# Kernel tuning notes

Measured on AMD Instinct MI355X. Metric: run time of the kernel, lower is better.

## Reference

```python
import jax, jax.numpy as jnp
import numpy as np

D_MODEL = 96
N_HEAD = 3
HEAD_DIM = D_MODEL // N_HEAD  # 32
D_FF = 2048
WIDTH = 65
HALF_W = (WIDTH - 1) // 2  # 32
EPS = 1e-5


def layer_norm(x, g, b):
    mu = jnp.mean(x, axis=-1, keepdims=True)
    var = jnp.mean(jnp.square(x - mu), axis=-1, keepdims=True)
    return (x - mu) * jax.lax.rsqrt(var + EPS) * g + b


def setup_inputs() -> dict:
    key = jax.random.key(0)
    ks = jax.random.split(key, 8)
    B, T = 8, 2048
    s = 0.05
    return {
        "x": jax.random.normal(ks[0], (B, D_MODEL, T), dtype=jnp.float32),
        "w_qkv": jax.random.normal(ks[1], (3 * D_MODEL, D_MODEL), dtype=jnp.float32) * s,
        "b_qkv": jnp.zeros((3 * D_MODEL,), dtype=jnp.float32),
        "w_out": jax.random.normal(ks[2], (D_MODEL, D_MODEL), dtype=jnp.float32) * s,
        "b_out": jnp.zeros((D_MODEL,), dtype=jnp.float32),
        "ln1_g": jnp.ones((D_MODEL,), dtype=jnp.float32),
        "ln1_b": jnp.zeros((D_MODEL,), dtype=jnp.float32),
        "w_ff1": jax.random.normal(ks[3], (D_FF, D_MODEL), dtype=jnp.float32) * s,
        "b_ff1": jnp.zeros((D_FF,), dtype=jnp.float32),
        "w_ff2": jax.random.normal(ks[4], (D_MODEL, D_FF), dtype=jnp.float32) * s,
        "b_ff2": jnp.zeros((D_MODEL,), dtype=jnp.float32),
        "ln2_g": jnp.ones((D_MODEL,), dtype=jnp.float32),
        "ln2_b": jnp.zeros((D_MODEL,), dtype=jnp.float32),
        "lnf_g": jnp.ones((D_MODEL,), dtype=jnp.float32),
        "lnf_b": jnp.zeros((D_MODEL,), dtype=jnp.float32),
    }


def reference(x, w_qkv, b_qkv, w_out, b_out, ln1_g, ln1_b, w_ff1, b_ff1,
              w_ff2, b_ff2, ln2_g, ln2_b, lnf_g, lnf_b):
    # x: (B, C, T) -> (B, T, C)
    h = jnp.transpose(x, (0, 2, 1))
    B, T, C = h.shape

    # --- multi-head self-attention with banded mask ---
    qkv = h @ w_qkv.T + b_qkv                      # (B, T, 3C)
    q, k, v = jnp.split(qkv, 3, axis=-1)
    q = q.reshape(B, T, N_HEAD, HEAD_DIM)
    k = k.reshape(B, T, N_HEAD, HEAD_DIM)
    v = v.reshape(B, T, N_HEAD, HEAD_DIM)

    scale = 1.0 / jnp.sqrt(jnp.float32(HEAD_DIM))
    scores = jnp.einsum("bthd,bshd->bhts", q, k) * scale  # (B, H, T, T)

    idx = jnp.arange(T)
    band = jnp.abs(idx[:, None] - idx[None, :]) <= HALF_W  # |i-j| <= half width
    scores = jnp.where(band[None, None], scores, jnp.float32(-jnp.inf))

    attn = jax.nn.softmax(scores, axis=-1)
    ctx = jnp.einsum("bhts,bshd->bthd", attn, v).reshape(B, T, C)
    attn_out = ctx @ w_out.T + b_out

    # --- post-norm encoder layer (dropout inactive / eval mode) ---
    h = layer_norm(h + attn_out, ln1_g, ln1_b)
    ff = jax.nn.relu(h @ w_ff1.T + b_ff1) @ w_ff2.T + b_ff2
    h = layer_norm(h + ff, ln2_g, ln2_b)

    # extra layernorm applied when width is not None
    h = layer_norm(h, lnf_g, lnf_b)

    # (B, T, C) -> (B, C, T)
    return jnp.transpose(h, (0, 2, 1))
```

## Files before the change

kernel.cpp:

```cpp
#include <hip/hip_runtime.h>
#include <hip/hip_bf16.h>

#define B 8
#define T 2048
#define C 96
#define NH 3
#define HD 32
#define FFD 2048
#define HALF_W 32
#define BT (B*T)

typedef __hip_bfloat16 bf16;
typedef __attribute__((ext_vector_type(8))) short short8;
typedef __attribute__((ext_vector_type(4))) short short4v;
typedef __attribute__((ext_vector_type(16))) float floatx16;

__device__ __forceinline__ short f2bs(float v){
    __hip_bfloat16 h = __float2bfloat16(v);
    return *reinterpret_cast<short*>(&h);
}
__device__ __forceinline__ float bs2f(short s){
    unsigned u = ((unsigned)(unsigned short)s) << 16;
    return __uint_as_float(u);
}
__device__ __forceinline__ short8 ld_b64x2(const short* p){
    short4v a = *(const short4v*)p;
    short4v b = *(const short4v*)(p + 4);
    short8 v;
    v[0]=a[0]; v[1]=a[1]; v[2]=a[2]; v[3]=a[3];
    v[4]=b[0]; v[5]=b[1]; v[6]=b[2]; v[7]=b[3];
    return v;
}
__device__ __forceinline__ int4 exch_pair(int a0,int a1,int b0,int b1,int hq){
    int ra0=__shfl_xor(a0,32), ra1=__shfl_xor(a1,32);
    int rb0=__shfl_xor(b0,32), rb1=__shfl_xor(b1,32);
    int4 s;
    s.x = hq ? rb0 : a0;
    s.y = hq ? rb1 : a1;
    s.z = hq ? b0  : ra0;
    s.w = hq ? b1  : ra1;
    return s;
}
__device__ __forceinline__ void proj_pack(const floatx16& acc, const float* bias32, int hq,
                                          short8& f0, short8& f1){
    int pkq[4][2];
    #pragma unroll
    for(int q = 0; q < 4; ++q){
        float4 bv = *(const float4*)(bias32 + 8*q + 4*hq);
        short4v t;
        t[0]=f2bs(acc[4*q+0]+bv.x); t[1]=f2bs(acc[4*q+1]+bv.y);
        t[2]=f2bs(acc[4*q+2]+bv.z); t[3]=f2bs(acc[4*q+3]+bv.w);
        int2 u = *(int2*)&t; pkq[q][0]=u.x; pkq[q][1]=u.y;
    }
    int4 r0 = exch_pair(pkq[0][0],pkq[0][1],pkq[1][0],pkq[1][1],hq);
    int4 r1 = exch_pair(pkq[2][0],pkq[2][1],pkq[3][0],pkq[3][1],hq);
    f0 = *(short8*)&r0; f1 = *(short8*)&r1;
}

__global__ void cvtw_kernel(const float* __restrict__ wq, const float* __restrict__ wo,
                            const float* __restrict__ w1, const float* __restrict__ w2,
                            bf16* __restrict__ dst){
    int i = blockIdx.x*256 + threadIdx.x;
    if(i < 27648){
        int e = i&7, lane = (i>>3)&63, r = i>>9;
        int ks = r%6, ot = r/6;
        int o = ot*32 + (lane&31);
        int k = ks*16 + (lane>>5)*8 + e;
        dst[i] = __float2bfloat16(wq[o*96 + k]);
    } else if(i < 36864){
        int j = i - 27648;
        int e = j&7, lane = (j>>3)&63, r = j>>9;
        int ks = r%6, ct = r/6;
        int c = ct*32 + (lane&31);
        int k = ks*16 + (lane>>5)*8 + e;
        dst[i] = __float2bfloat16(wo[c*96 + k]);
    } else if(i < 233472){
        int j = i - 36864;
        int e = j&7, lane = (j>>3)&63, r = j>>9;
        int ks = r%6; r /= 6;
        int w = r%4, jt = r/4;
        int row = jt*128 + w*32 + (lane&31);
        int k = ks*16 + (lane>>5)*8 + e;
        dst[i] = __float2bfloat16(w1[row*96 + k]);
    } else if(i < 430080){
        int j = i - 233472;
        int e = j&7, lane = (j>>3)&63, r = j>>9;
        int ct = r%3; r /= 3;
        int g = r%2; r /= 2;
        int w = r%4, jt = r/4;
        int c = ct*32 + (lane&31);
        int k = jt*128 + w*32 + g*16 + (lane>>5)*8 + e;
        dst[i] = __float2bfloat16(w2[c*FFD + k]);
    }
}

__global__ __launch_bounds__(192, 2) void encoder_kernel(
    const float* __restrict__ x,
    const bf16* __restrict__ wqs, const bf16* __restrict__ wos,
    const bf16* __restrict__ w1s, const bf16* __restrict__ w2s,
    const float* __restrict__ b_qkv, const float* __restrict__ b_out,
    const float* __restrict__ g1, const float* __restrict__ bb1,
    const float* __restrict__ b1, const float* __restrict__ b2,
    const float* __restrict__ g2, const float* __restrict__ bt2,
    const float* __restrict__ gf, const float* __restrict__ btf,
    float* __restrict__ out){
    __shared__ __align__(16) char smem[73088];
    float* XS   = (float*)smem;
    short* PTS  = (short*)smem;
    float* REDP = (float*)smem;
    short* VTS  = (short*)(smem + 39936);
    float* ZT   = (float*)(smem + 39936);
    short* CTX  = (short*)(smem + 59136);
    short* H1S  = (short*)(smem + 65536);
    float* LSS  = (float*)(smem + 71936);
    float* RED1 = (float*)(smem + 72320);

    const int tid = threadIdx.x;
    const int w = tid / 64, lane = tid & 63;
    const int lm = lane & 31, hq = lane >> 5;
    const int b  = blockIdx.x >> 6;
    const int tt = blockIdx.x & 63;
    const int t0 = tt * 32;
    const float* xb = x + (size_t)b*C*T;

    short8 wof[6];
    #pragma unroll
    for(int ks = 0; ks < 6; ++ks)
        wof[ks] = *(const short8*)((const short*)wos + (size_t)(w*6 + ks)*512 + lane*8);

    int tg0 = t0 - 32;
    if(tg0 >= 0 && t0 + 64 <= T){
        for(int e = tid; e < 96*24; e += 192){
            int c = e / 24, q4 = e % 24;
            *(float4*)(XS + c*104 + q4*4) = *(const float4*)(xb + (size_t)c*T + tg0 + q4*4);
        }
    } else {
        for(int e = tid; e < 96*96; e += 192){
            int c = e / 96, j = e % 96;
            int t = tg0 + j; t = t < 0 ? 0 : (t > T-1 ? T-1 : t);
            XS[c*104 + j] = xb[(size_t)c*T + t];
        }
    }
    __syncthreads();

    short8 kwf[6], vwf[6];
    #pragma unroll
    for(int ks = 0; ks < 6; ++ks){
        kwf[ks] = *(const short8*)((const short*)wqs + (size_t)((3+w)*6 + ks)*512 + lane*8);
        vwf[ks] = *(const short8*)((const short*)wqs + (size_t)((6+w)*6 + ks)*512 + lane*8);
    }
    short8 kf[3][2]; short8 qf0, qf1;
    #pragma unroll
    for(int tau = 0; tau < 3; ++tau){
        short8 bfr[6];
        #pragma unroll
        for(int ks = 0; ks < 6; ++ks){
            short8 vv;
            #pragma unroll
            for(int i = 0; i < 8; ++i)
                vv[i] = f2bs(XS[(ks*16 + hq*8 + i)*104 + tau*32 + lm]);
            bfr[ks] = vv;
        }
        floatx16 acc;
        #pragma unroll
        for(int r = 0; r < 16; ++r) acc[r] = 0.f;
        #pragma unroll
        for(int ks = 0; ks < 6; ++ks)
            acc = __builtin_amdgcn_mfma_f32_32x32x16_bf16(kwf[ks], bfr[ks], acc, 0,0,0);
        proj_pack(acc, b_qkv + (3+w)*32, hq, kf[tau][0], kf[tau][1]);
        #pragma unroll
        for(int r = 0; r < 16; ++r) acc[r] = 0.f;
        #pragma unroll
        for(int ks = 0; ks < 6; ++ks)
            acc = __builtin_amdgcn_mfma_f32_32x32x16_bf16(vwf[ks], bfr[ks], acc, 0,0,0);
        #pragma unroll
        for(int q = 0; q < 4; ++q){
            float4 bv = *(const float4*)(b_qkv + (6+w)*32 + 8*q + 4*hq);
            float bva[4] = {bv.x, bv.y, bv.z, bv.w};
            #pragma unroll
            for(int r = 0; r < 4; ++r)
                VTS[w*3200 + (8*q + 4*hq + r)*100 + tau*32 + lm] = f2bs(acc[4*q+r] + bva[r]);
        }
        if(tau == 1){
            floatx16 qa;
            #pragma unroll
            for(int r = 0; r < 16; ++r) qa[r] = 0.f;
            #pragma unroll
            for(int ks = 0; ks < 6; ++ks){
                short8 qwf = *(const short8*)((const short*)wqs + (size_t)(w*6 + ks)*512 + lane*8);
                qa = __builtin_amdgcn_mfma_f32_32x32x16_bf16(qwf, bfr[ks], qa, 0,0,0);
            }
            proj_pack(qa, b_qkv + w*32, hq, qf0, qf1);
        }
    }
    __syncthreads();

    floatx16 S[3];
    #pragma unroll
    for(int sub = 0; sub < 3; ++sub){
        floatx16 z;
        #pragma unroll
        for(int r = 0; r < 16; ++r) z[r] = 0.f;
        z = __builtin_amdgcn_mfma_f32_32x32x16_bf16(kf[sub][0], qf0, z, 0,0,0);
        z = __builtin_amdgcn_mfma_f32_32x32x16_bf16(kf[sub][1], qf1, z, 0,0,0);
        S[sub] = z;
    }
    const float scale = 0.17677669529663687f;
    float part = 0.f;
    #pragma unroll
    for(int sub = 0; sub < 3; ++sub){
        #pragma unroll
        for(int r = 0; r < 16; ++r){
            int key_local = sub*32 + (r&3) + 8*(r>>2) + 4*hq;
            int s_glob = t0 - 32 + key_local;
            int rel = key_local - lm;
            bool ok = (rel >= 0) && (rel <= 64) && (s_glob >= 0) && (s_glob < T);
            float p = ok ? __expf(S[sub][r]*scale) : 0.f;
            S[sub][r] = p;
            part += p;
        }
    }
    float ltot = part + __shfl_xor(part, 32);
    if(hq == 0) LSS[w*32 + lm] = ltot;
    #pragma unroll
    for(int sub = 0; sub < 3; ++sub){
        #pragma unroll
        for(int q4 = 0; q4 < 4; ++q4){
            int kbase = sub*32 + 8*q4 + 4*hq;
            short4v pk4;
            pk4[0] = f2bs(S[sub][4*q4+0]);
            pk4[1] = f2bs(S[sub][4*q4+1]);
            pk4[2] = f2bs(S[sub][4*q4+2]);
            pk4[3] = f2bs(S[sub][4*q4+3]);
            *(short4v*)(PTS + w*3200 + lm*100 + kbase) = pk4;
        }
    }
    floatx16 O;
    #pragma unroll
    for(int r = 0; r < 16; ++r) O[r] = 0.f;
    #pragma unroll
    for(int ks = 0; ks < 6; ++ks){
        short8 pa = ld_b64x2(PTS + w*3200 + lm*100 + ks*16 + hq*8);
        short8 vf = ld_b64x2(VTS + w*3200 + lm*100 + ks*16 + hq*8);
        O = __builtin_amdgcn_mfma_f32_32x32x16_bf16(pa, vf, O, 0,0,0);
    }
    #pragma unroll
    for(int r = 0; r < 16; ++r){
        int qr = (r&3) + 8*(r>>2) + 4*hq;
        float linv = 1.f / LSS[w*32 + qr];
        CTX[qr*100 + w*32 + lm] = f2bs(O[r]*linv);
    }
    __syncthreads();

    short8 cbfr[6];
    #pragma unroll
    for(int ks = 0; ks < 6; ++ks)
        cbfr[ks] = ld_b64x2(CTX + lm*100 + ks*16 + hq*8);
    floatx16 pacc;
    #pragma unroll
    for(int r = 0; r < 16; ++r) pacc[r] = 0.f;
    #pragma unroll
    for(int ks = 0; ks < 6; ++ks)
        pacc = __builtin_amdgcn_mfma_f32_32x32x16_bf16(wof[ks], cbfr[ks], pacc, 0,0,0);
    float vals[16];
    float p1 = 0.f, p2 = 0.f;
    #pragma unroll
    for(int q = 0; q < 4; ++q){
        int c = w*32 + 8*q + 4*hq;
        float4 bv = *(const float4*)(b_out + c);
        float bva[4] = {bv.x, bv.y, bv.z, bv.w};
        #pragma unroll
        for(int r = 0; r < 4; ++r){
            float xv = xb[(size_t)(c + r)*T + t0 + lm];
            float v = pacc[4*q+r] + bva[r] + xv;
            vals[4*q+r] = v;
            p1 += v; p2 += v*v;
        }
    }
    p1 += __shfl_xor(p1, 32);
    p2 += __shfl_xor(p2, 32);
    if(hq == 0){ RED1[w*32 + lm] = p1; RED1[96 + w*32 + lm] = p2; }
    __syncthreads();
    {
        float s  = RED1[lm] + RED1[32 + lm] + RED1[64 + lm];
        float s2 = RED1[96 + lm] + RED1[128 + lm] + RED1[160 + lm];
        float mu = s * (1.0f/96.0f);
        float rstd = rsqrtf(s2*(1.0f/96.0f) - mu*mu + 1e-5f);
        #pragma unroll
        for(int q = 0; q < 4; ++q){
            int c = w*32 + 8*q + 4*hq;
            float4 gv = *(const float4*)(g1 + c);
            float4 bv = *(const float4*)(bb1 + c);
            float ga[4] = {gv.x, gv.y, gv.z, gv.w};
            float ba[4] = {bv.x, bv.y, bv.z, bv.w};
            short4v pkv;
            #pragma unroll
            for(int r = 0; r < 4; ++r)
                pkv[r] = f2bs((vals[4*q+r] - mu)*rstd*ga[r] + ba[r]);
            *(short4v*)(H1S + lm*100 + c) = pkv;
        }
    }
    __syncthreads();

    short8 hf[6];
    #pragma unroll
    for(int ks = 0; ks < 6; ++ks)
        hf[ks] = ld_b64x2(H1S + lm*100 + ks*16 + hq*8);
    floatx16 acc2[3];
    #pragma unroll
    for(int i = 0; i < 3; ++i)
        #pragma unroll
        for(int r = 0; r < 16; ++r) acc2[i][r] = 0.f;
    const short* w1b = (const short*)w1s + lane*8;
    const short* w2b = (const short*)w2s + lane*8;
    short8 cw1[6], cw2[6];
    #pragma unroll
    for(int ks = 0; ks < 6; ++ks)
        cw1[ks] = *(const short8*)(w1b + (size_t)(w*6 + ks)*512);
    #pragma unroll
    for(int g = 0; g < 2; ++g)
        #pragma unroll
        for(int ct = 0; ct < 3; ++ct)
            cw2[g*3 + ct] = *(const short8*)(w2b + (size_t)((w*2 + g)*3 + ct)*512);
    for(int J = w; J < 64; J += 3){
        int Jn = (J + 3 < 64) ? J + 3 : w;
        short8 nw1[6], nw2[6];
        #pragma unroll
        for(int ks = 0; ks < 6; ++ks)
            nw1[ks] = *(const short8*)(w1b + (size_t)(Jn*6 + ks)*512);
        #pragma unroll
        for(int g = 0; g < 2; ++g)
            #pragma unroll
            for(int ct = 0; ct < 3; ++ct)
                nw2[g*3 + ct] = *(const short8*)(w2b + (size_t)((Jn*2 + g)*3 + ct)*512);
        floatx16 a0;
        #pragma unroll
        for(int r = 0; r < 16; ++r) a0[r] = 0.f;
        #pragma unroll
        for(int ks = 0; ks < 6; ++ks)
            a0 = __builtin_amdgcn_mfma_f32_32x32x16_bf16(cw1[ks], hf[ks], a0, 0,0,0);
        int pk[4][2];
        #pragma unroll
        for(int q = 0; q < 4; ++q){
            float4 bv = *(const float4*)(b1 + J*32 + 8*q + 4*hq);
            float bva[4] = {bv.x, bv.y, bv.z, bv.w};
            short4v tv;
            #pragma unroll
            for(int r = 0; r < 4; ++r){
                float v0 = a0[4*q+r] + bva[r];
                tv[r] = f2bs(v0 > 0.f ? v0 : 0.f);
            }
            int2 u = *(int2*)&tv; pk[q][0] = u.x; pk[q][1] = u.y;
        }
        #pragma unroll
        for(int g = 0; g < 2; ++g){
            int4 sfi = exch_pair(pk[2*g][0], pk[2*g][1], pk[2*g+1][0], pk[2*g+1][1], hq);
            short8 sf = *(short8*)&sfi;
            #pragma unroll
            for(int ct = 0; ct < 3; ++ct)
                acc2[ct] = __builtin_amdgcn_mfma_f32_32x32x16_bf16(cw2[g*3+ct], sf, acc2[ct], 0,0,0);
        }
        #pragma unroll
        for(int ks = 0; ks < 6; ++ks) cw1[ks] = nw1[ks];
        #pragma unroll
        for(int i = 0; i < 6; ++i) cw2[i] = nw2[i];
    }
    #pragma unroll
    for(int ct = 0; ct < 3; ++ct)
        #pragma unroll
        for(int q = 0; q < 4; ++q)
            #pragma unroll
            for(int r = 0; r < 4; ++r)
                REDP[(w*3 + ct)*1088 + lane*17 + 4*q + r] = acc2[ct][4*q+r];
    __syncthreads();

    float fv[16];
    float e1 = 0.f, e2 = 0.f;
    #pragma unroll
    for(int q = 0; q < 4; ++q){
        int c = w*32 + 8*q + 4*hq;
        float4 bv = *(const float4*)(b2 + c);
        float bva[4] = {bv.x, bv.y, bv.z, bv.w};
        #pragma unroll
        for(int r = 0; r < 4; ++r){
            float v = REDP[(0 + w)*1088 + lane*17 + 4*q + r]
                    + REDP[(3 + w)*1088 + lane*17 + 4*q + r]
                    + REDP[(6 + w)*1088 + lane*17 + 4*q + r]
                    + bva[r] + bs2f(H1S[lm*100 + c + r]);
            fv[4*q+r] = v;
            e1 += v; e2 += v*v;
        }
    }
    e1 += __shfl_xor(e1, 32);
    e2 += __shfl_xor(e2, 32);
    if(hq == 0){ RED1[w*32 + lm] = e1; RED1[96 + w*32 + lm] = e2; }
    __syncthreads();
    float f1 = 0.f, f2 = 0.f;
    {
        float s  = RED1[lm] + RED1[32 + lm] + RED1[64 + lm];
        float s2 = RED1[96 + lm] + RED1[128 + lm] + RED1[160 + lm];
        float mu = s * (1.0f/96.0f);
        float rstd = rsqrtf(s2*(1.0f/96.0f) - mu*mu + 1e-5f);
        #pragma unroll
        for(int q = 0; q < 4; ++q){
            int c = w*32 + 8*q + 4*hq;
            float4 gv = *(const float4*)(g2 + c);
            float4 bv = *(const float4*)(bt2 + c);
            float ga[4] = {gv.x, gv.y, gv.z, gv.w};
            float ba[4] = {bv.x, bv.y, bv.z, bv.w};
            #pragma unroll
            for(int r = 0; r < 4; ++r){
                float y = (fv[4*q+r] - mu)*rstd*ga[r] + ba[r];
                fv[4*q+r] = y;
                f1 += y; f2 += y*y;
            }
        }
    }
    f1 += __shfl_xor(f1, 32);
    f2 += __shfl_xor(f2, 32);
    __syncthreads();
    if(hq == 0){ RED1[w*32 + lm] = f1; RED1[96 + w*32 + lm] = f2; }
    __syncthreads();
    {
        float s  = RED1[lm] + RED1[32 + lm] + RED1[64 + lm];
        float s2 = RED1[96 + lm] + RED1[128 + lm] + RED1[160 + lm];
        float mu = s * (1.0f/96.0f);
        float rstd = rsqrtf(s2*(1.0f/96.0f) - mu*mu + 1e-5f);
        #pragma unroll
        for(int q = 0; q < 4; ++q){
            int c = w*32 + 8*q + 4*hq;
            float4 gv = *(const float4*)(gf + c);
            float4 bv = *(const float4*)(btf + c);
            float ga[4] = {gv.x, gv.y, gv.z, gv.w};
            float ba[4] = {bv.x, bv.y, bv.z, bv.w};
            #pragma unroll
            for(int r = 0; r < 4; ++r)
                ZT[(c + r)*36 + lm] = (fv[4*q+r] - mu)*rstd*ga[r] + ba[r];
        }
    }
    __syncthreads();
    float* ob = out + (size_t)b*C*T + t0;
    for(int e = tid; e < 96*8; e += 192){
        int c = e >> 3, qq = e & 7;
        *(float4*)(ob + (size_t)c*T + qq*4) = *(const float4*)(ZT + c*36 + qq*4);
    }
}

extern "C" void kernel_launch(void* const* d_in, const int* in_sizes, int n_in,
                              void* d_out, int out_size, void* d_ws, size_t ws_size,
                              hipStream_t stream) {
    const float* x     = (const float*)d_in[0];
    const float* w_qkv = (const float*)d_in[1];
    const float* b_qkv = (const float*)d_in[2];
    const float* w_out = (const float*)d_in[3];
    const float* b_out = (const float*)d_in[4];
    const float* ln1_g = (const float*)d_in[5];
    const float* ln1_b = (const float*)d_in[6];
    const float* w_ff1 = (const float*)d_in[7];
    const float* b_ff1 = (const float*)d_in[8];
    const float* w_ff2 = (const float*)d_in[9];
    const float* b_ff2 = (const float*)d_in[10];
    const float* ln2_g = (const float*)d_in[11];
    const float* ln2_b = (const float*)d_in[12];
    const float* lnf_g = (const float*)d_in[13];
    const float* lnf_b = (const float*)d_in[14];
    float* out = (float*)d_out;

    bf16* wts = (bf16*)d_ws;
    bf16* wqs = wts;
    bf16* wos = wts + 27648;
    bf16* w1s = wts + 36864;
    bf16* w2s = wts + 233472;

    cvtw_kernel   <<<1680, 256, 0, stream>>>(w_qkv, w_out, w_ff1, w_ff2, wts);
    encoder_kernel<<<B*(T/32), 192, 0, stream>>>(x, wqs, wos, w1s, w2s,
                                                 b_qkv, b_out, ln1_g, ln1_b,
                                                 b_ff1, b_ff2, ln2_g, ln2_b,
                                                 lnf_g, lnf_b, out);
}
```

Measured before the change: 124.6 us.

## Double block to six waves, split K/V projection and FFN chunks across waves

Raises the block size from 3 to 6 wavefronts. In the projection stage, three waves compute Q/K and three compute V. All six waves share the FFN hidden-chunk loop, and the six partial FFN2 accumulators are reduced through shared memory one channel tile at a time. X is staged in LDS as bf16 in time-major layout so MFMA operands load as vectors, which shrinks shared memory. This adds more barriers and leaves half the waves idle during attention and the layernorms, in exchange for more waves to hide latency in the FFN-dominated section.

```diff
diff --git a/kernel.cpp b/kernel.cpp
--- a/kernel.cpp
+++ b/kernel.cpp
@@ -9,6 +9,7 @@
 #define FFD 2048
 #define HALF_W 32
 #define BT (B*T)
+#define NT 384
 
 typedef __hip_bfloat16 bf16;
 typedef __attribute__((ext_vector_type(8))) short short8;
@@ -94,7 +95,7 @@
     }
 }
 
-__global__ __launch_bounds__(192, 2) void encoder_kernel(
+__global__ __launch_bounds__(384, 3) void encoder_kernel(
     const float* __restrict__ x,
     const bf16* __restrict__ wqs, const bf16* __restrict__ wos,
     const bf16* __restrict__ w1s, const bf16* __restrict__ w2s,
@@ -104,191 +105,206 @@
     const float* __restrict__ g2, const float* __restrict__ bt2,
     const float* __restrict__ gf, const float* __restrict__ btf,
     float* __restrict__ out){
-    __shared__ __align__(16) char smem[73088];
-    float* XS   = (float*)smem;
+    __shared__ __align__(16) char smem[59392];
+    short* XS   = (short*)smem;
     short* PTS  = (short*)smem;
     float* REDP = (float*)smem;
-    short* VTS  = (short*)(smem + 39936);
-    float* ZT   = (float*)(smem + 39936);
-    short* CTX  = (short*)(smem + 59136);
-    short* H1S  = (short*)(smem + 65536);
-    float* LSS  = (float*)(smem + 71936);
-    float* RED1 = (float*)(smem + 72320);
+    short* VTS  = (short*)(smem + 26112);
+    float* ZT   = (float*)(smem + 26112);
+    short* CTX  = (short*)(smem + 45312);
+    short* H1S  = (short*)(smem + 51712);
+    float* LSS  = (float*)(smem + 58112);
+    float* RED1 = (float*)(smem + 58496);
 
     const int tid = threadIdx.x;
-    const int w = tid / 64, lane = tid & 63;
+    const int u = tid >> 6, lane = tid & 63;
     const int lm = lane & 31, hq = lane >> 5;
+    const int grp = u / 3, h = u % 3;
     const int b  = blockIdx.x >> 6;
     const int tt = blockIdx.x & 63;
     const int t0 = tt * 32;
     const float* xb = x + (size_t)b*C*T;
 
-    short8 wof[6];
-    #pragma unroll
-    for(int ks = 0; ks < 6; ++ks)
-        wof[ks] = *(const short8*)((const short*)wos + (size_t)(w*6 + ks)*512 + lane*8);
-
     int tg0 = t0 - 32;
     if(tg0 >= 0 && t0 + 64 <= T){
-        for(int e = tid; e < 96*24; e += 192){
-            int c = e / 24, q4 = e % 24;
-            *(float4*)(XS + c*104 + q4*4) = *(const float4*)(xb + (size_t)c*T + tg0 + q4*4);
+        for(int e = tid; e < 96*24; e += NT){
+            int c = e / 24, t4 = e % 24;
+            float4 v = *(const float4*)(xb + (size_t)c*T + tg0 + t4*4);
+            XS[(t4*4+0)*104 + c] = f2bs(v.x);
+            XS[(t4*4+1)*104 + c] = f2bs(v.y);
+            XS[(t4*4+2)*104 + c] = f2bs(v.z);
+            XS[(t4*4+3)*104 + c] = f2bs(v.w);
         }
     } else {
-        for(int e = tid; e < 96*96; e += 192){
+        for(int e = tid; e < 96*96; e += NT){
             int c = e / 96, j = e % 96;
             int t = tg0 + j; t = t < 0 ? 0 : (t > T-1 ? T-1 : t);
-            XS[c*104 + j] = xb[(size_t)c*T + t];
-        }
-    }
-    __syncthreads();
-
-    short8 kwf[6], vwf[6];
-    #pragma unroll
-    for(int ks = 0; ks < 6; ++ks){
-        kwf[ks] = *(const short8*)((const short*)wqs + (size_t)((3+w)*6 + ks)*512 + lane*8);
-        vwf[ks] = *(const short8*)((const short*)wqs + (size_t)((6+w)*6 + ks)*512 + lane*8);
-    }
-    short8 kf[3][2]; short8 qf0, qf1;
-    #pragma unroll
-    for(int tau = 0; tau < 3; ++tau){
-        short8 bfr[6];
+            XS[j*104 + c] = f2bs(xb[(size_t)c*T + t]);
+        }
+    }
+    __syncthreads();
+
+    short8 kf[3][2], qf0, qf1, wof[6];
+    if(grp == 0){
+        short8 kwf[6];
+        #pragma unroll
+        for(int ks = 0; ks < 6; ++ks)
+            kwf[ks] = *(const short8*)((const short*)wqs + (size_t)((3+h)*6 + ks)*512 + lane*8);
+        #pragma unroll
+        for(int tau = 0; tau < 3; ++tau){
+            short8 bfr[6];
+            #pragma unroll
+            for(int ks = 0; ks < 6; ++ks)
+                bfr[ks] = *(const short8*)(XS + (tau*32+lm)*104 + ks*16 + hq*8);
+            floatx16 acc;
+            #pragma unroll
+            for(int r = 0; r < 16; ++r) acc[r] = 0.f;
+            #pragma unroll
+            for(int ks = 0; ks < 6; ++ks)
+                acc = __builtin_amdgcn_mfma_f32_32x32x16_bf16(kwf[ks], bfr[ks], acc, 0,0,0);
+            proj_pack(acc, b_qkv + (3+h)*32, hq, kf[tau][0], kf[tau][1]);
+            if(tau == 1){
+                floatx16 qa;
+                #pragma unroll
+                for(int r = 0; r < 16; ++r) qa[r] = 0.f;
+                #pragma unroll
+                for(int ks = 0; ks < 6; ++ks){
+                    short8 qwf = *(const short8*)((const short*)wqs + (size_t)(h*6 + ks)*512 + lane*8);
+                    qa = __builtin_amdgcn_mfma_f32_32x32x16_bf16(qwf, bfr[ks], qa, 0,0,0);
+                }
+                proj_pack(qa, b_qkv + h*32, hq, qf0, qf1);
+            }
+        }
+        #pragma unroll
+        for(int ks = 0; ks < 6; ++ks)
+            wof[ks] = *(const short8*)((const short*)wos + (size_t)(h*6 + ks)*512 + lane*8);
+    } else {
+        short8 vwf[6];
+        #pragma unroll
+        for(int ks = 0; ks < 6; ++ks)
+            vwf[ks] = *(const short8*)((const short*)wqs + (size_t)((6+h)*6 + ks)*512 + lane*8);
+        #pragma unroll
+        for(int tau = 0; tau < 3; ++tau){
+            short8 bfr[6];
+            #pragma unroll
+            for(int ks = 0; ks < 6; ++ks)
+                bfr[ks] = *(const short8*)(XS + (tau*32+lm)*104 + ks*16 + hq*8);
+            floatx16 acc;
+            #pragma unroll
+            for(int r = 0; r < 16; ++r) acc[r] = 0.f;
+            #pragma unroll
+            for(int ks = 0; ks < 6; ++ks)
+                acc = __builtin_amdgcn_mfma_f32_32x32x16_bf16(vwf[ks], bfr[ks], acc, 0,0,0);
+            #pragma unroll
+            for(int q = 0; q < 4; ++q){
+                float4 bv = *(const float4*)(b_qkv + (6+h)*32 + 8*q + 4*hq);
+                float bva[4] = {bv.x, bv.y, bv.z, bv.w};
+                #pragma unroll
+                for(int r = 0; r < 4; ++r)
+                    VTS[h*3200 + (8*q + 4*hq + r)*100 + tau*32 + lm] = f2bs(acc[4*q+r] + bva[r]);
+            }
+        }
+    }
+    __syncthreads();
+
+    if(grp == 0){
+        floatx16 S[3];
+        #pragma unroll
+        for(int sub = 0; sub < 3; ++sub){
+            floatx16 z;
+            #pragma unroll
+            for(int r = 0; r < 16; ++r) z[r] = 0.f;
+            z = __builtin_amdgcn_mfma_f32_32x32x16_bf16(kf[sub][0], qf0, z, 0,0,0);
+            z = __builtin_amdgcn_mfma_f32_32x32x16_bf16(kf[sub][1], qf1, z, 0,0,0);
+            S[sub] = z;
+        }
+        const float scale = 0.17677669529663687f;
+        float part = 0.f;
+        #pragma unroll
+        for(int sub = 0; sub < 3; ++sub){
+            #pragma unroll
+            for(int r = 0; r < 16; ++r){
+                int key_local = sub*32 + (r&3) + 8*(r>>2) + 4*hq;
+                int s_glob = t0 - 32 + key_local;
+                int rel = key_local - lm;
+                bool ok = (rel >= 0) && (rel <= 64) && (s_glob >= 0) && (s_glob < T);
+                float p = ok ? __expf(S[sub][r]*scale) : 0.f;
+                S[sub][r] = p;
+                part += p;
+            }
+        }
+        float ltot = part + __shfl_xor(part, 32);
+        if(hq == 0) LSS[h*32 + lm] = ltot;
+        #pragma unroll
+        for(int sub = 0; sub < 3; ++sub){
+            #pragma unroll
+            for(int q4 = 0; q4 < 4; ++q4){
+                int kbase = sub*32 + 8*q4 + 4*hq;
+                short4v pk4;
+                pk4[0] = f2bs(S[sub][4*q4+0]);
+                pk4[1] = f2bs(S[sub][4*q4+1]);
+                pk4[2] = f2bs(S[sub][4*q4+2]);
+                pk4[3] = f2bs(S[sub][4*q4+3]);
+                *(short4v*)(PTS + h*3200 + lm*100 + kbase) = pk4;
+            }
+        }
+        floatx16 O;
+        #pragma unroll
+        for(int r = 0; r < 16; ++r) O[r] = 0.f;
         #pragma unroll
         for(int ks = 0; ks < 6; ++ks){
-            short8 vv;
-            #pragma unroll
-            for(int i = 0; i < 8; ++i)
-                vv[i] = f2bs(XS[(ks*16 + hq*8 + i)*104 + tau*32 + lm]);
-            bfr[ks] = vv;
-        }
-        floatx16 acc;
-        #pragma unroll
-        for(int r = 0; r < 16; ++r) acc[r] = 0.f;
-        #pragma unroll
-        for(int ks = 0; ks < 6; ++ks)
-            acc = __builtin_amdgcn_mfma_f32_32x32x16_bf16(kwf[ks], bfr[ks], acc, 0,0,0);
-        proj_pack(acc, b_qkv + (3+w)*32, hq, kf[tau][0], kf[tau][1]);
-        #pragma unroll
-        for(int r = 0; r < 16; ++r) acc[r] = 0.f;
-        #pragma unroll
-        for(int ks = 0; ks < 6; ++ks)
-            acc = __builtin_amdgcn_mfma_f32_32x32x16_bf16(vwf[ks], bfr[ks], acc, 0,0,0);
+            short8 pa = ld_b64x2(PTS + h*3200 + lm*100 + ks*16 + hq*8);
+            short8 vf = ld_b64x2(VTS + h*3200 + lm*100 + ks*16 + hq*8);
+            O = __builtin_amdgcn_mfma_f32_32x32x16_bf16(pa, vf, O, 0,0,0);
+        }
+        #pragma unroll
+        for(int r = 0; r < 16; ++r){
+            int qr = (r&3) + 8*(r>>2) + 4*hq;
+            float linv = 1.f / LSS[h*32 + qr];
+            CTX[qr*100 + h*32 + lm] = f2bs(O[r]*linv);
+        }
+    }
+    __syncthreads();
+
+    float vals[16];
+    if(grp == 0){
+        short8 cbfr[6];
+        #pragma unroll
+        for(int ks = 0; ks < 6; ++ks)
+            cbfr[ks] = ld_b64x2(CTX + lm*100 + ks*16 + hq*8);
+        floatx16 pacc;
+        #pragma unroll
+        for(int r = 0; r < 16; ++r) pacc[r] = 0.f;
+        #pragma unroll
+        for(int ks = 0; ks < 6; ++ks)
+            pacc = __builtin_amdgcn_mfma_f32_32x32x16_bf16(wof[ks], cbfr[ks], pacc, 0,0,0);
+        float p1 = 0.f, p2 = 0.f;
         #pragma unroll
         for(int q = 0; q < 4; ++q){
-            float4 bv = *(const float4*)(b_qkv + (6+w)*32 + 8*q + 4*hq);
+            int c = h*32 + 8*q + 4*hq;
+            float4 bv = *(const float4*)(b_out + c);
             float bva[4] = {bv.x, bv.y, bv.z, bv.w};
             #pragma unroll
-            for(int r = 0; r < 4; ++r)
-                VTS[w*3200 + (8*q + 4*hq + r)*100 + tau*32 + lm] = f2bs(acc[4*q+r] + bva[r]);
-        }
-        if(tau == 1){
-            floatx16 qa;
-            #pragma unroll
-            for(int r = 0; r < 16; ++r) qa[r] = 0.f;
-            #pragma unroll
-            for(int ks = 0; ks < 6; ++ks){
-                short8 qwf = *(const short8*)((const short*)wqs + (size_t)(w*6 + ks)*512 + lane*8);
-                qa = __builtin_amdgcn_mfma_f32_32x32x16_bf16(qwf, bfr[ks], qa, 0,0,0);
-            }
-            proj_pack(qa, b_qkv + w*32, hq, qf0, qf1);
-        }
-    }
-    __syncthreads();
-
-    floatx16 S[3];
-    #pragma unroll
-    for(int sub = 0; sub < 3; ++sub){
-        floatx16 z;
-        #pragma unroll
-        for(int r = 0; r < 16; ++r) z[r] = 0.f;
-        z = __builtin_amdgcn_mfma_f32_32x32x16_bf16(kf[sub][0], qf0, z, 0,0,0);
-        z = __builtin_amdgcn_mfma_f32_32x32x16_bf16(kf[sub][1], qf1, z, 0,0,0);
-        S[sub] = z;
-    }
-    const float scale = 0.17677669529663687f;
-    float part = 0.f;
-    #pragma unroll
-    for(int sub = 0; sub < 3; ++sub){
-        #pragma unroll
-        for(int r = 0; r < 16; ++r){
-            int key_local = sub*32 + (r&3) + 8*(r>>2) + 4*hq;
-            int s_glob = t0 - 32 + key_local;
-            int rel = key_local - lm;
-            bool ok = (rel >= 0) && (rel <= 64) && (s_glob >= 0) && (s_glob < T);
-            float p = ok ? __expf(S[sub][r]*scale) : 0.f;
-            S[sub][r] = p;
-            part += p;
-        }
-    }
-    float ltot = part + __shfl_xor(part, 32);
-    if(hq == 0) LSS[w*32 + lm] = ltot;
-    #pragma unroll
-    for(int sub = 0; sub < 3; ++sub){
-        #pragma unroll
-        for(int q4 = 0; q4 < 4; ++q4){
-            int kbase = sub*32 + 8*q4 + 4*hq;
-            short4v pk4;
-            pk4[0] = f2bs(S[sub][4*q4+0]);
-            pk4[1] = f2bs(S[sub][4*q4+1]);
-            pk4[2] = f2bs(S[sub][4*q4+2]);
-            pk4[3] = f2bs(S[sub][4*q4+3]);
-            *(short4v*)(PTS + w*3200 + lm*100 + kbase) = pk4;
-        }
-    }
-    floatx16 O;
-    #pragma unroll
-    for(int r = 0; r < 16; ++r) O[r] = 0.f;
-    #pragma unroll
-    for(int ks = 0; ks < 6; ++ks){
-        short8 pa = ld_b64x2(PTS + w*3200 + lm*100 + ks*16 + hq*8);
-        short8 vf = ld_b64x2(VTS + w*3200 + lm*100 + ks*16 + hq*8);
-        O = __builtin_amdgcn_mfma_f32_32x32x16_bf16(pa, vf, O, 0,0,0);
-    }
-    #pragma unroll
-    for(int r = 0; r < 16; ++r){
-        int qr = (r&3) + 8*(r>>2) + 4*hq;
-        float linv = 1.f / LSS[w*32 + qr];
-        CTX[qr*100 + w*32 + lm] = f2bs(O[r]*linv);
-    }
-    __syncthreads();
-
-    short8 cbfr[6];
-    #pragma unroll
-    for(int ks = 0; ks < 6; ++ks)
-        cbfr[ks] = ld_b64x2(CTX + lm*100 + ks*16 + hq*8);
-    floatx16 pacc;
-    #pragma unroll
-    for(int r = 0; r < 16; ++r) pacc[r] = 0.f;
-    #pragma unroll
-    for(int ks = 0; ks < 6; ++ks)
-        pacc = __builtin_amdgcn_mfma_f32_32x32x16_bf16(wof[ks], cbfr[ks], pacc, 0,0,0);
-    float vals[16];
-    float p1 = 0.f, p2 = 0.f;
-    #pragma unroll
-    for(int q = 0; q < 4; ++q){
-        int c = w*32 + 8*q + 4*hq;
-        float4 bv = *(const float4*)(b_out + c);
-        float bva[4] = {bv.x, bv.y, bv.z, bv.w};
-        #pragma unroll
-        for(int r = 0; r < 4; ++r){
-            float xv = xb[(size_t)(c + r)*T + t0 + lm];
-            float v = pacc[4*q+r] + bva[r] + xv;
-            vals[4*q+r] = v;
-            p1 += v; p2 += v*v;
-        }
-    }
-    p1 += __shfl_xor(p1, 32);
-    p2 += __shfl_xor(p2, 32);
-    if(hq == 0){ RED1[w*32 + lm] = p1; RED1[96 + w*32 + lm] = p2; }
-    __syncthreads();
-    {
+            for(int r = 0; r < 4; ++r){
+                float xv = xb[(size_t)(c + r)*T + t0 + lm];
+                float v = pacc[4*q+r] + bva[r] + xv;
+                vals[4*q+r] = v;
+                p1 += v; p2 += v*v;
+            }
+        }
+        p1 += __shfl_xor(p1, 32);
+        p2 += __shfl_xor(p2, 32);
+        if(hq == 0){ RED1[h*32 + lm] = p1; RED1[96 + h*32 + lm] = p2; }
+    }
+    __syncthreads();
+    if(grp == 0){
         float s  = RED1[lm] + RED1[32 + lm] + RED1[64 + lm];
         float s2 = RED1[96 + lm] + RED1[128 + lm] + RED1[160 + lm];
         float mu = s * (1.0f/96.0f);
         float rstd = rsqrtf(s2*(1.0f/96.0f) - mu*mu + 1e-5f);
         #pragma unroll
         for(int q = 0; q < 4; ++q){
-            int c = w*32 + 8*q + 4*hq;
+            int c = h*32 + 8*q + 4*hq;
             float4 gv = *(const float4*)(g1 + c);
             float4 bv = *(const float4*)(bb1 + c);
             float ga[4] = {gv.x, gv.y, gv.z, gv.w};
@@ -313,26 +329,24 @@
         for(int r = 0; r < 16; ++r) acc2[i][r] = 0.f;
     const short* w1b = (const short*)w1s + lane*8;
     const short* w2b = (const short*)w2s + lane*8;
-    short8 cw1[6], cw2[6];
+    short8 cw1[6];
     #pragma unroll
     for(int ks = 0; ks < 6; ++ks)
-        cw1[ks] = *(const short8*)(w1b + (size_t)(w*6 + ks)*512);
-    #pragma unroll
-    for(int g = 0; g < 2; ++g)
-        #pragma unroll
-        for(int ct = 0; ct < 3; ++ct)
-            cw2[g*3 + ct] = *(const short8*)(w2b + (size_t)((w*2 + g)*3 + ct)*512);
-    for(int J = w; J < 64; J += 3){
-        int Jn = (J + 3 < 64) ? J + 3 : w;
-        short8 nw1[6], nw2[6];
+        cw1[ks] = *(const short8*)(w1b + (size_t)(u*6 + ks)*512);
+    const int nJ = (u < 4) ? 11 : 10;
+    for(int it = 0; it < nJ; ++it){
+        const int J  = u + it*6;
+        const int Jn = (J + 6 < 64) ? J + 6 : u;
+        short8 nw1[6];
         #pragma unroll
         for(int ks = 0; ks < 6; ++ks)
             nw1[ks] = *(const short8*)(w1b + (size_t)(Jn*6 + ks)*512);
+        short8 w2f[6];
         #pragma unroll
         for(int g = 0; g < 2; ++g)
             #pragma unroll
             for(int ct = 0; ct < 3; ++ct)
-                nw2[g*3 + ct] = *(const short8*)(w2b + (size_t)((Jn*2 + g)*3 + ct)*512);
+                w2f[g*3 + ct] = *(const short8*)(w2b + (size_t)((J*2 + g)*3 + ct)*512);
         floatx16 a0;
         #pragma unroll
         for(int r = 0; r < 16; ++r) a0[r] = 0.f;
@@ -350,7 +364,7 @@
                 float v0 = a0[4*q+r] + bva[r];
                 tv[r] = f2bs(v0 > 0.f ? v0 : 0.f);
             }
-            int2 u = *(int2*)&tv; pk[q][0] = u.x; pk[q][1] = u.y;
+            int2 uu = *(int2*)&tv; pk[q][0] = uu.x; pk[q][1] = uu.y;
         }
         #pragma unroll
         for(int g = 0; g < 2; ++g){
@@ -358,52 +372,58 @@
             short8 sf = *(short8*)&sfi;
             #pragma unroll
             for(int ct = 0; ct < 3; ++ct)
-                acc2[ct] = __builtin_amdgcn_mfma_f32_32x32x16_bf16(cw2[g*3+ct], sf, acc2[ct], 0,0,0);
+                acc2[ct] = __builtin_amdgcn_mfma_f32_32x32x16_bf16(w2f[g*3+ct], sf, acc2[ct], 0,0,0);
         }
         #pragma unroll
         for(int ks = 0; ks < 6; ++ks) cw1[ks] = nw1[ks];
-        #pragma unroll
-        for(int i = 0; i < 6; ++i) cw2[i] = nw2[i];
-    }
-    #pragma unroll
-    for(int ct = 0; ct < 3; ++ct)
-        #pragma unroll
-        for(int q = 0; q < 4; ++q)
-            #pragma unroll
-            for(int r = 0; r < 4; ++r)
-                REDP[(w*3 + ct)*1088 + lane*17 + 4*q + r] = acc2[ct][4*q+r];
-    __syncthreads();
+    }
 
     float fv[16];
     float e1 = 0.f, e2 = 0.f;
-    #pragma unroll
-    for(int q = 0; q < 4; ++q){
-        int c = w*32 + 8*q + 4*hq;
-        float4 bv = *(const float4*)(b2 + c);
-        float bva[4] = {bv.x, bv.y, bv.z, bv.w};
-        #pragma unroll
-        for(int r = 0; r < 4; ++r){
-            float v = REDP[(0 + w)*1088 + lane*17 + 4*q + r]
-                    + REDP[(3 + w)*1088 + lane*17 + 4*q + r]
-                    + REDP[(6 + w)*1088 + lane*17 + 4*q + r]
-                    + bva[r] + bs2f(H1S[lm*100 + c + r]);
-            fv[4*q+r] = v;
-            e1 += v; e2 += v*v;
-        }
-    }
-    e1 += __shfl_xor(e1, 32);
-    e2 += __shfl_xor(e2, 32);
-    if(hq == 0){ RED1[w*32 + lm] = e1; RED1[96 + w*32 + lm] = e2; }
+    for(int s = 0; s < 3; ++s){
+        #pragma unroll
+        for(int q = 0; q < 4; ++q)
+            #pragma unroll
+            for(int r = 0; r < 4; ++r)
+                REDP[u*1088 + lane*17 + 4*q + r] = acc2[s][4*q+r];
+        __syncthreads();
+        if(u == s){
+            #pragma unroll
+            for(int q = 0; q < 4; ++q){
+                int c = s*32 + 8*q + 4*hq;
+                float4 bv = *(const float4*)(b2 + c);
+                float bva[4] = {bv.x, bv.y, bv.z, bv.w};
+                #pragma unroll
+                for(int r = 0; r < 4; ++r){
+                    float v = REDP[0*1088 + lane*17 + 4*q + r]
+                            + REDP[1*1088 + lane*17 + 4*q + r]
+                            + REDP[2*1088 + lane*17 + 4*q + r]
+                            + REDP[3*1088 + lane*17 + 4*q + r]
+                            + REDP[4*1088 + lane*17 + 4*q + r]
+                            + REDP[5*1088 + lane*17 + 4*q + r]
+                            + bva[r] + bs2f(H1S[lm*100 + c + r]);
+                    fv[4*q+r] = v;
+                    e1 += v; e2 += v*v;
+                }
+            }
+        }
+        __syncthreads();
+    }
+    if(grp == 0){
+        e1 += __shfl_xor(e1, 32);
+        e2 += __shfl_xor(e2, 32);
+        if(hq == 0){ RED1[h*32 + lm] = e1; RED1[96 + h*32 + lm] = e2; }
+    }
     __syncthreads();
     float f1 = 0.f, f2 = 0.f;
-    {
+    if(grp == 0){
         float s  = RED1[lm] + RED1[32 + lm] + RED1[64 + lm];
         float s2 = RED1[96 + lm] + RED1[128 + lm] + RED1[160 + lm];
         float mu = s * (1.0f/96.0f);
         float rstd = rsqrtf(s2*(1.0f/96.0f) - mu*mu + 1e-5f);
         #pragma unroll
         for(int q = 0; q < 4; ++q){
-            int c = w*32 + 8*q + 4*hq;
+            int c = h*32 + 8*q + 4*hq;
             float4 gv = *(const float4*)(g2 + c);
             float4 bv = *(const float4*)(bt2 + c);
             float ga[4] = {gv.x, gv.y, gv.z, gv.w};
@@ -415,20 +435,20 @@
                 f1 += y; f2 += y*y;
             }
         }
-    }
-    f1 += __shfl_xor(f1, 32);
-    f2 += __shfl_xor(f2, 32);
-    __syncthreads();
-    if(hq == 0){ RED1[w*32 + lm] = f1; RED1[96 + w*32 + lm] = f2; }
-    __syncthreads();
-    {
+        f1 += __shfl_xor(f1, 32);
+        f2 += __shfl_xor(f2, 32);
+    }
+    __syncthreads();
+    if(grp == 0 && hq == 0){ RED1[h*32 + lm] = f1; RED1[96 + h*32 + lm] = f2; }
+    __syncthreads();
+    if(grp == 0){
         float s  = RED1[lm] + RED1[32 + lm] + RED1[64 + lm];
         float s2 = RED1[96 + lm] + RED1[128 + lm] + RED1[160 + lm];
         float mu = s * (1.0f/96.0f);
         float rstd = rsqrtf(s2*(1.0f/96.0f) - mu*mu + 1e-5f);
         #pragma unroll
         for(int q = 0; q < 4; ++q){
-            int c = w*32 + 8*q + 4*hq;
+            int c = h*32 + 8*q + 4*hq;
             float4 gv = *(const float4*)(gf + c);
             float4 bv = *(const float4*)(btf + c);
             float ga[4] = {gv.x, gv.y, gv.z, gv.w};
@@ -440,7 +460,7 @@
     }
     __syncthreads();
     float* ob = out + (size_t)b*C*T + t0;
-    for(int e = tid; e < 96*8; e += 192){
+    for(int e = tid; e < 96*8; e += NT){
         int c = e >> 3, qq = e & 7;
         *(float4*)(ob + (size_t)c*T + qq*4) = *(const float4*)(ZT + c*36 + qq*4);
     }
@@ -473,8 +493,8 @@
     bf16* w2s = wts + 233472;
 
     cvtw_kernel   <<<1680, 256, 0, stream>>>(w_qkv, w_out, w_ff1, w_ff2, wts);
-    encoder_kernel<<<B*(T/32), 192, 0, stream>>>(x, wqs, wos, w1s, w2s,
-                                                 b_qkv, b_out, ln1_g, ln1_b,
-                                                 b_ff1, b_ff2, ln2_g, ln2_b,
-                                                 lnf_g, lnf_b, out);
-}
+    encoder_kernel<<<B*(T/32), NT, 0, stream>>>(x, wqs, wos, w1s, w2s,
+                                                b_qkv, b_out, ln1_g, ln1_b,
+                                                b_ff1, b_ff2, ln2_g, ln2_b,
+                                                lnf_g, lnf_b, out);
+}
```

Measured after the change: 135.7 us. +8.9%, slower.
